# Kernel optimization log

Hardware: AMD Instinct MI355X
Metric: run time of the kernel (lower is better)

The kernel has to match this reference:

```python
import jax, jax.numpy as jnp
import numpy as np
from jax import lax

H = 384
W = 384
N = H * W                 # flattened pixel count
N_LOC = N // 2            # unknown pixels with 3x3 matting-Laplacian stencils
KCM = 20                  # color-mixture KNN size
K_IU = 5                  # intra-unknown KNN size
NNZ_CM = N_LOC * KCM


def setup_inputs() -> dict:
    key = jax.random.key(0)
    ks = jax.random.split(key, 16)
    f32 = jnp.float32
    i32 = jnp.int32
    inp = {}
    inp["CM_weights"] = jax.random.uniform(ks[0], (N,), f32)
    inp["LOC_weights"] = jax.random.uniform(ks[1], (N,), f32)
    inp["IU_weights"] = jax.random.uniform(ks[2], (N,), f32)
    inp["KU_weights"] = jax.random.uniform(ks[3], (N,), f32)
    inp["lmbda"] = jnp.full((1,), 100.0, f32)
    inp["kToUconf"] = jax.random.uniform(ks[4], (N,), f32)
    inp["known"] = jax.random.uniform(ks[5], (N,), f32)
    inp["kToU"] = jax.random.uniform(ks[6], (N,), f32)
    inp["Wcm_data"] = jax.random.uniform(ks[7], (NNZ_CM,), f32)
    inp["LOC_flows"] = jax.random.uniform(ks[8], (9, 9, N_LOC), f32)
    inp["IU_flows"] = jax.random.uniform(ks[9], (N_LOC, K_IU), f32)
    inp["Wcm_row"] = jax.random.randint(ks[10], (NNZ_CM,), 0, N, dtype=i32)
    inp["Wcm_col"] = jax.random.randint(ks[11], (NNZ_CM,), 0, N, dtype=i32)
    # interior pixels so all 9 stencil neighbours are valid
    inp["LOC_inInd"] = jax.random.randint(ks[12], (N_LOC,), W + 1, N - W - 1, dtype=i32)
    inp["IU_inInd"] = jax.random.randint(ks[13], (N_LOC,), 0, N, dtype=i32)
    inp["IU_neighInd"] = jax.random.randint(ks[14], (N_LOC, K_IU), 0, N, dtype=i32)
    inp["width"] = W
    inp["cg_steps"] = 30
    return inp


def reference(CM_weights, LOC_weights, IU_weights, KU_weights, lmbda,
              kToUconf, known, kToU, Wcm_data, LOC_flows, IU_flows,
              Wcm_row, Wcm_col, LOC_inInd, IU_inInd, IU_neighInd,
              width, cg_steps):
    n = kToU.shape[0]
    seg = lambda v, i: jax.ops.segment_sum(v, i, num_segments=n)

    # --- color mixture: Wcm scaled by diag(CM_weights); L = diag(rowsum) - Wcm; Lcm = L^T L
    cm_vals = CM_weights[Wcm_row] * Wcm_data
    rs_cm = seg(cm_vals, Wcm_row)

    # --- matting Laplacian: 9x9 flows per unknown pixel over 3x3 stencil
    offs = jnp.array([-1 - width, -1, -1 + width, -width, 0, width,
                      1 - width, 1, 1 + width], dtype=LOC_inInd.dtype)
    neigh = LOC_inInd[:, None] + offs[None, :]                    # [n_loc, 9]
    fl = LOC_flows * LOC_weights[LOC_inInd][None, None, :]        # [9, 9, n_loc]
    nloc = neigh.shape[0]
    # entry (row=neigh[k,i], col=neigh[k,j]) has value fl[j, i, k]
    vals_m = jnp.transpose(fl, (2, 1, 0)).reshape(-1)
    rows_m = jnp.broadcast_to(neigh[:, :, None], (nloc, 9, 9)).reshape(-1)
    cols_m = jnp.broadcast_to(neigh[:, None, :], (nloc, 9, 9)).reshape(-1)
    rows_ms = jnp.concatenate([rows_m, cols_m])
    cols_ms = jnp.concatenate([cols_m, rows_m])
    vals_ms = 0.5 * jnp.concatenate([vals_m, vals_m])             # W = 0.5 (W + W^T)
    rs_m = seg(vals_ms, rows_ms)

    # --- intra-unknowns KNN affinities
    fiu = IU_flows * IU_weights[IU_inInd][:, None]                # [n_iu, K]
    rows_c0 = jnp.broadcast_to(IU_inInd[:, None], IU_neighInd.shape).reshape(-1)
    cols_c0 = IU_neighInd.reshape(-1)
    rows_cs = jnp.concatenate([rows_c0, cols_c0])
    cols_cs = jnp.concatenate([cols_c0, rows_c0])
    vals_cs = 0.5 * jnp.concatenate([fiu.reshape(-1), fiu.reshape(-1)])
    rs_c = seg(vals_cs, rows_cs)

    # --- diagonal data terms: KU + lmbda*known
    diag_ku = KU_weights * kToUconf + lmbda[0] * known
    b = diag_ku * kToU

    def matvec(v):
        # Lcm @ v = L^T (L v), keeping L in factored COO form
        Lv = rs_cm * v - seg(cm_vals * v[Wcm_col], Wcm_row)
        lcm = rs_cm * Lv - seg(cm_vals * Lv[Wcm_row], Wcm_col)
        lm = rs_m * v - seg(vals_ms * v[cols_ms], rows_ms)
        lc = rs_c * v - seg(vals_cs * v[cols_cs], rows_cs)
        return lcm + lm + lc + diag_ku * v

    def cg_step(carry, _):
        x, r, p, rs = carry
        Ap = matvec(p)
        alpha = rs / jnp.vdot(p, Ap)
        x = x + alpha * p
        r = r - alpha * Ap
        rs_new = jnp.vdot(r, r)
        p = r + (rs_new / rs) * p
        return (x, r, p, rs_new), None

    x0 = jnp.zeros_like(b)  # x0 = 0 as in MattingSolver
    (x, _, _, _), _ = lax.scan(cg_step, (x0, b, b, jnp.vdot(b, b)), None, length=cg_steps)
    return x
```

## Files before the change

### kernel.cpp

```cpp
#include <hip/hip_runtime.h>


#define TPB 256

__device__ __forceinline__ float blockReduce256(float v) {
  #pragma unroll
  for (int o = 32; o > 0; o >>= 1) v += __shfl_down(v, o, 64);
  __shared__ float s[4];
  int lane = threadIdx.x & 63, wv = threadIdx.x >> 6;
  if (lane == 0) s[wv] = v;
  __syncthreads();
  return (threadIdx.x == 0) ? (s[0] + s[1] + s[2] + s[3]) : 0.f;
}

__global__ void k_init0(const float* __restrict__ KUw, const float* __restrict__ kToUconf,
                        const float* __restrict__ lmbda, const float* __restrict__ known,
                        const float* __restrict__ kToU,
                        float* __restrict__ diag_ku, float2* __restrict__ PR,
                        float* __restrict__ x,
                        int* __restrict__ CNT, int* __restrict__ sCNT,
                        float* __restrict__ scal, int N)
{
  int i = blockIdx.x * TPB + threadIdx.x;
  if (i < 80) scal[i] = 0.f;
  if (i < 576) sCNT[i] = 0;
  if (i < 3 * N) CNT[i] = 0;
  float red = 0.f;
  if (i < N) {
    float dk = KUw[i] * kToUconf[i] + lmbda[0] * known[i];
    diag_ku[i] = dk;
    float b = dk * kToU[i];
    PR[i] = make_float2(b, b);
    x[i] = 0.f;
    red = b * b;
  }
  float v = blockReduce256(red);
  if (threadIdx.x == 0) atomicAdd(&scal[0], v);
}

__global__ void k_prep(float* __restrict__ LOC_flows, const int* __restrict__ LOC_inInd,
                       const float* __restrict__ LOCw, int NLOC)
{
  int k = blockIdx.x * TPB + threadIdx.x;
  float Fl[81];
  #pragma unroll
  for (int m = 0; m < 81; ++m) Fl[m] = LOC_flows[(size_t)m * NLOC + k];
  float hw = 0.5f * LOCw[LOC_inInd[k]];
  int idx = 0;
  #pragma unroll
  for (int a = 0; a < 9; ++a)
    #pragma unroll
    for (int b = a + 1; b < 9; ++b) {
      LOC_flows[(size_t)idx * NLOC + k] = hw * (Fl[a * 9 + b] + Fl[b * 9 + a]);
      ++idx;
    }
}

__global__ void k_sh(const int* __restrict__ LOC_inInd, int* __restrict__ sCNT,
                     unsigned short* __restrict__ sTick, int NLOC)
{
  int k = blockIdx.x * TPB + threadIdx.x;
  sTick[k] = (unsigned short)atomicAdd(&sCNT[LOC_inInd[k] >> 8], 1);
}

__global__ void k_ss(int* __restrict__ sCNT)
{
  __shared__ int s[576];
  int v = sCNT[threadIdx.x];
  s[threadIdx.x] = v;
  __syncthreads();
  for (int o = 1; o < 576; o <<= 1) {
    int t = (threadIdx.x >= o) ? s[threadIdx.x - o] : 0;
    __syncthreads();
    s[threadIdx.x] += t;
    __syncthreads();
  }
  sCNT[threadIdx.x] = s[threadIdx.x] - v;
}

__global__ void k_sc(const int* __restrict__ LOC_inInd, const int* __restrict__ sCNT,
                     const unsigned short* __restrict__ sTick,
                     int* __restrict__ perm, int* __restrict__ LOC_inIndP, int NLOC)
{
  int k = blockIdx.x * TPB + threadIdx.x;
  int v = LOC_inInd[k];
  int pos = sCNT[v >> 8] + sTick[k];
  perm[pos] = k;
  LOC_inIndP[pos] = v;
}

__global__ void k_permS2(float* __restrict__ LOC_flows, const int* __restrict__ perm,
                         int NLOC)
{
  int kp = blockIdx.x * TPB + threadIdx.x;
  int k = perm[kp];
  #pragma unroll
  for (int m = 0; m < 36; ++m)
    LOC_flows[(size_t)(36 + m) * NLOC + kp] = LOC_flows[(size_t)m * NLOC + k];
}

__global__ void k_hist(const int* __restrict__ Wrow, const int* __restrict__ Wcol,
                       const int* __restrict__ LOC_inIndP, const int* __restrict__ width_p,
                       const int* __restrict__ IU_inInd, const int* __restrict__ IU_neighInd,
                       int* __restrict__ CNT,
                       unsigned short* __restrict__ tr, unsigned short* __restrict__ tc,
                       unsigned short* __restrict__ tU,
                       int NLOC, int N, int B0, int B1)
{
  int blk = blockIdx.x;
  if (blk < B0) {
    int e = blk * TPB + threadIdx.x;
    tr[e] = (unsigned short)atomicAdd(&CNT[Wrow[e]], 1);
    tc[e] = (unsigned short)atomicAdd(&CNT[N + Wcol[e]], 1);
  } else if (blk < B1) {
    int kp = (blk - B0) * TPB + threadIdx.x;
    int wd = *width_p;
    int base = LOC_inIndP[kp];
    const int offs[9] = {-1 - wd, -1, -1 + wd, -wd, 0, wd, 1 - wd, 1, 1 + wd};
    #pragma unroll
    for (int a = 0; a < 9; ++a)
      tU[a * NLOC + kp] = (unsigned short)atomicAdd(&CNT[2 * N + base + offs[a]], 1);
  } else {
    int k = (blk - B1) * TPB + threadIdx.x;
    tU[14 * NLOC + k] = (unsigned short)atomicAdd(&CNT[2 * N + IU_inInd[k]], 1);
    #pragma unroll
    for (int j = 0; j < 5; ++j)
      tU[(9 + j) * NLOC + k] =
          (unsigned short)atomicAdd(&CNT[2 * N + IU_neighInd[k * 5 + j]], 1);
  }
}

__global__ void k_scan1(int* __restrict__ OFF, int* __restrict__ bsum, int tot)
{
  __shared__ int s[TPB];
  int gid = blockIdx.x * TPB + threadIdx.x;
  int v = (gid < tot) ? OFF[gid] : 0;
  s[threadIdx.x] = v;
  __syncthreads();
  #pragma unroll
  for (int o = 1; o < TPB; o <<= 1) {
    int t = (threadIdx.x >= o) ? s[threadIdx.x - o] : 0;
    __syncthreads();
    s[threadIdx.x] += t;
    __syncthreads();
  }
  if (gid < tot) OFF[gid] = s[threadIdx.x] - v;
  if (threadIdx.x == TPB - 1) bsum[blockIdx.x] = s[threadIdx.x];
}

__global__ void k_scan2(int* __restrict__ bsum, int nPerArr)
{
  __shared__ int s[1024];
  int base = blockIdx.x * nPerArr;
  int v = (threadIdx.x < nPerArr) ? bsum[base + threadIdx.x] : 0;
  s[threadIdx.x] = v;
  __syncthreads();
  for (int o = 1; o < 1024; o <<= 1) {
    int t = (threadIdx.x >= o) ? s[threadIdx.x - o] : 0;
    __syncthreads();
    s[threadIdx.x] += t;
    __syncthreads();
  }
  if (threadIdx.x < nPerArr) bsum[base + threadIdx.x] = s[threadIdx.x] - v;
}

__global__ void k_scan3(int* __restrict__ OFF, const int* __restrict__ bsum, int tot)
{
  int gid = blockIdx.x * TPB + threadIdx.x;
  if (gid < tot) OFF[gid] += bsum[blockIdx.x];
}

__global__ void k_fill(const float* __restrict__ CMw, const float* __restrict__ Wcm_data,
                       const int* __restrict__ Wrow, const int* __restrict__ Wcol,
                       const int* __restrict__ LOC_inIndP, const int* __restrict__ width_p,
                       const int* __restrict__ IU_inInd, const int* __restrict__ IU_neighInd,
                       const int* __restrict__ OFF,
                       const unsigned short* __restrict__ tr, const unsigned short* __restrict__ tc,
                       const unsigned short* __restrict__ tU,
                       int2* __restrict__ csrPk, int2* __restrict__ cscPk,
                       int* __restrict__ gU,
                       int NLOC, int N, int B0, int B1)
{
  int blk = blockIdx.x;
  if (blk < B0) {
    int e = blk * TPB + threadIdx.x;
    int row = Wrow[e], col = Wcol[e];
    int cv = __float_as_int(CMw[row] * Wcm_data[e]);
    csrPk[OFF[row] + tr[e]] = make_int2(col, cv);
    cscPk[OFF[N + col] + tc[e]] = make_int2(row, cv);
  } else if (blk < B1) {
    int kp = (blk - B0) * TPB + threadIdx.x;
    int wd = *width_p;
    int base = LOC_inIndP[kp];
    const int offs[9] = {-1 - wd, -1, -1 + wd, -wd, 0, wd, 1 - wd, 1, 1 + wd};
    #pragma unroll
    for (int a = 0; a < 9; ++a)
      gU[OFF[2 * N + base + offs[a]] + tU[a * NLOC + kp]] = a * NLOC + kp;
  } else {
    int k = (blk - B1) * TPB + threadIdx.x;
    gU[OFF[2 * N + IU_inInd[k]] + tU[14 * NLOC + k]] = 14 * NLOC + k;
    #pragma unroll
    for (int j = 0; j < 5; ++j)
      gU[OFF[2 * N + IU_neighInd[k * 5 + j]] + tU[(9 + j) * NLOC + k]] =
          (9 + j) * NLOC + k;
  }
}

__global__ void k_it1(const float2* __restrict__ PR,
                      const float* __restrict__ S2p, const int* __restrict__ LOC_inIndP,
                      const int* __restrict__ width_p,
                      const float* __restrict__ IU_flows, const int* __restrict__ IU_inInd,
                      const int* __restrict__ IU_neighInd, const float* __restrict__ IUw,
                      const float* __restrict__ diag_ku,
                      const int* __restrict__ OFF, const int2* __restrict__ csrPk,
                      float* __restrict__ u_all,
                      float* __restrict__ Lv, float* __restrict__ rs_cm,
                      const float* __restrict__ rsN, const float* __restrict__ rsO, int first,
                      float* __restrict__ pAp_t,
                      int NNZ, int NLOC, int N, int B0, int B1)
{
  int blk = blockIdx.x;
  float beta = first ? 0.f : rsN[0] / rsO[0];
  float red = 0.f;
  if (blk < B0) {
    int kp = blk * TPB + threadIdx.x;
    int wd = *width_p;
    int base = LOC_inIndP[kp];
    const int offs[9] = {-1 - wd, -1, -1 + wd, -wd, 0, wd, 1 - wd, 1, 1 + wd};
    float pv[9];
    #pragma unroll
    for (int a = 0; a < 9; ++a) {
      float2 pr = PR[base + offs[a]];
      pv[a] = __builtin_fmaf(beta, pr.x, pr.y);
    }
    float u[9] = {0.f, 0.f, 0.f, 0.f, 0.f, 0.f, 0.f, 0.f, 0.f};
    float qf = 0.f;
    int idx = 0;
    #pragma unroll
    for (int a = 0; a < 9; ++a)
      #pragma unroll
      for (int b = a + 1; b < 9; ++b) {
        float sv = S2p[(size_t)idx * NLOC + kp];
        ++idx;
        float d = pv[a] - pv[b];
        float t = sv * d;
        u[a] += t; u[b] -= t;
        qf += t * d;
      }
    #pragma unroll
    for (int a = 0; a < 9; ++a) u_all[a * NLOC + kp] = u[a];
    red = qf;
  } else if (blk < B1) {
    int k = (blk - B0) * TPB + threadIdx.x;
    int r0 = IU_inInd[k];
    float hw = 0.5f * IUw[r0];
    float2 prr = PR[r0];
    float pr = __builtin_fmaf(beta, prr.x, prr.y);
    int c[5]; float w[5];
    #pragma unroll
    for (int j = 0; j < 5; ++j) {
      c[j] = IU_neighInd[k * 5 + j];
      w[j] = hw * IU_flows[k * 5 + j];
    }
    float pc[5];
    #pragma unroll
    for (int j = 0; j < 5; ++j) {
      float2 pp = PR[c[j]];
      pc[j] = __builtin_fmaf(beta, pp.x, pp.y);
    }
    float qf = 0.f, asum = 0.f;
    #pragma unroll
    for (int j = 0; j < 5; ++j) {
      float d = pr - pc[j];
      float uA = w[j] * d;
      u_all[(9 + j) * NLOC + k] = -uA;
      asum += uA;
      qf += uA * d;
    }
    u_all[14 * NLOC + k] = asum;
    red = qf;
  } else {
    int i = (blk - B1) * TPB + threadIdx.x;
    float2 pri = PR[i];
    float pi = __builtin_fmaf(beta, pri.x, pri.y);
    int s = OFF[i];
    int e = (i == N - 1) ? NNZ : OFF[i + 1];
    float acc = 0.f, rs = 0.f;
    int q = s;
    for (; q + 8 <= e; q += 8) {
      int2 ed[8];
      #pragma unroll
      for (int m = 0; m < 8; ++m) ed[m] = csrPk[q + m];
      float g[8];
      #pragma unroll
      for (int m = 0; m < 8; ++m) {
        float2 pp = PR[ed[m].x];
        g[m] = __builtin_fmaf(beta, pp.x, pp.y);
      }
      #pragma unroll
      for (int m = 0; m < 8; ++m) {
        float cv = __int_as_float(ed[m].y);
        rs += cv;
        acc += cv * (pi - g[m]);
      }
    }
    for (; q + 4 <= e; q += 4) {
      int2 ed[4];
      #pragma unroll
      for (int m = 0; m < 4; ++m) ed[m] = csrPk[q + m];
      float g[4];
      #pragma unroll
      for (int m = 0; m < 4; ++m) {
        float2 pp = PR[ed[m].x];
        g[m] = __builtin_fmaf(beta, pp.x, pp.y);
      }
      #pragma unroll
      for (int m = 0; m < 4; ++m) {
        float cv = __int_as_float(ed[m].y);
        rs += cv;
        acc += cv * (pi - g[m]);
      }
    }
    for (; q < e; ++q) {
      int2 ed = csrPk[q];
      float cv = __int_as_float(ed.y);
      float2 pp = PR[ed.x];
      rs += cv;
      acc += cv * (pi - __builtin_fmaf(beta, pp.x, pp.y));
    }
    Lv[i] = acc;
    rs_cm[i] = rs;
    red = diag_ku[i] * pi * pi + acc * acc;
  }
  float v = blockReduce256(red);
  if (threadIdx.x == 0) atomicAdd(pAp_t, v);
}

__global__ void k_it2(float* __restrict__ x, float2* __restrict__ PR,
                      const float* __restrict__ Lv,
                      const float* __restrict__ rs_cm, const float* __restrict__ diag_ku,
                      const int* __restrict__ OFF,
                      const int2* __restrict__ cscPk,
                      const int* __restrict__ gU, const float* __restrict__ u_all,
                      const float* __restrict__ rs_t, const float* __restrict__ pAp_t,
                      const float* __restrict__ rsO, int first,
                      float* __restrict__ rs_t1,
                      int NNZ, int NLOC, int N)
{
  int i = blockIdx.x * TPB + threadIdx.x;
  float alpha = rs_t[0] / pAp_t[0];
  float beta = first ? 0.f : rs_t[0] / rsO[0];
  float tg = 0.f;
  {
    int s0 = OFF[2 * N + i];
    int e0 = (i == N - 1) ? 15 * NLOC : OFF[2 * N + i + 1];
    int q = s0;
    for (; q + 8 <= e0; q += 8) {
      int g[8];
      #pragma unroll
      for (int m = 0; m < 8; ++m) g[m] = gU[q + m];
      float u[8];
      #pragma unroll
      for (int m = 0; m < 8; ++m) u[m] = u_all[g[m]];
      #pragma unroll
      for (int m = 0; m < 8; ++m) tg += u[m];
    }
    for (; q + 4 <= e0; q += 4) {
      int g[4];
      #pragma unroll
      for (int m = 0; m < 4; ++m) g[m] = gU[q + m];
      float u[4];
      #pragma unroll
      for (int m = 0; m < 4; ++m) u[m] = u_all[g[m]];
      #pragma unroll
      for (int m = 0; m < 4; ++m) tg += u[m];
    }
    for (; q < e0; ++q) tg += u_all[gU[q]];
  }
  float sc = 0.f;
  {
    int s0 = OFF[N + i];
    int e0 = (i == N - 1) ? NNZ : OFF[N + i + 1];
    int q = s0;
    for (; q + 8 <= e0; q += 8) {
      int2 ed[8];
      #pragma unroll
      for (int m = 0; m < 8; ++m) ed[m] = cscPk[q + m];
      float l[8];
      #pragma unroll
      for (int m = 0; m < 8; ++m) l[m] = Lv[ed[m].x];
      #pragma unroll
      for (int m = 0; m < 8; ++m) sc += __int_as_float(ed[m].y) * l[m];
    }
    for (; q + 4 <= e0; q += 4) {
      int2 ed[4];
      #pragma unroll
      for (int m = 0; m < 4; ++m) ed[m] = cscPk[q + m];
      float l[4];
      #pragma unroll
      for (int m = 0; m < 4; ++m) l[m] = Lv[ed[m].x];
      #pragma unroll
      for (int m = 0; m < 4; ++m) sc += __int_as_float(ed[m].y) * l[m];
    }
    for (; q < e0; ++q) {
      int2 ed = cscPk[q];
      sc += __int_as_float(ed.y) * Lv[ed.x];
    }
  }
  float2 pri = PR[i];
  float pi = __builtin_fmaf(beta, pri.x, pri.y);
  float Ap = diag_ku[i] * pi + rs_cm[i] * Lv[i] - sc + tg;
  x[i] += alpha * pi;
  float rn = pri.y - alpha * Ap;
  PR[i] = make_float2(pi, rn);
  float v = blockReduce256(rn * rn);
  if (threadIdx.x == 0) atomicAdd(rs_t1, v);
}

extern "C" void kernel_launch(void* const* d_in, const int* in_sizes, int n_in,
                              void* d_out, int out_size, void* d_ws, size_t ws_size,
                              hipStream_t stream)
{
  const float* CMw       = (const float*)d_in[0];
  const float* LOCw      = (const float*)d_in[1];
  const float* IUw       = (const float*)d_in[2];
  const float* KUw       = (const float*)d_in[3];
  const float* lmbda     = (const float*)d_in[4];
  const float* kToUconf  = (const float*)d_in[5];
  const float* known     = (const float*)d_in[6];
  const float* kToU      = (const float*)d_in[7];
  const float* Wcm_data  = (const float*)d_in[8];
  float*       LOC_flows = (float*)d_in[9];
  const float* IU_flows  = (const float*)d_in[10];
  const int*   Wrow      = (const int*)d_in[11];
  const int*   Wcol      = (const int*)d_in[12];
  const int*   LOC_inInd = (const int*)d_in[13];
  const int*   IU_inInd  = (const int*)d_in[14];
  const int*   IU_neighInd = (const int*)d_in[15];
  const int*   width_p   = (const int*)d_in[16];
  const int CG_STEPS = 30;

  const int N    = in_sizes[0];
  const int NNZ  = in_sizes[8];
  const int NLOC = in_sizes[13];

  float* x       = (float*)d_out;
  float2* PR     = (float2*)d_ws;
  float* Lv      = (float*)(PR + (size_t)N);
  float* rs_cm   = Lv + N;
  float* diag_ku = rs_cm + N;
  int2*  csrPk   = (int2*)(diag_ku + N);
  int2*  cscPk   = csrPk + (size_t)NNZ;
  int*   gU      = (int*)(cscPk + (size_t)NNZ);
  int*   OFF     = gU + (size_t)15 * NLOC;
  unsigned short* tr = (unsigned short*)(OFF + (size_t)3 * N);
  unsigned short* tc = tr + (size_t)NNZ;
  unsigned short* tU = tc + (size_t)NNZ;
  float* u_all   = (float*)tr;
  int*   bsum    = (int*)(tU + (size_t)15 * NLOC);
  float* scal    = (float*)(bsum + 3 * (N / TPB));
  int*   perm    = (int*)(scal + 80);
  int*   LOC_inIndP = perm + NLOC;
  int*   sCNT    = LOC_inIndP + NLOC;
  unsigned short* sTick = (unsigned short*)(sCNT + 576);

  const int Bn = N / TPB;
  const int Bz = NNZ / TPB;
  const int Bl = NLOC / TPB;
  const int Z3 = 3 * Bn;

  k_init0<<<Z3, TPB, 0, stream>>>(KUw, kToUconf, lmbda, known, kToU,
                                  diag_ku, PR, x, OFF, sCNT, scal, N);
  k_prep<<<Bl, TPB, 0, stream>>>(LOC_flows, LOC_inInd, LOCw, NLOC);
  k_sh<<<Bl, TPB, 0, stream>>>(LOC_inInd, sCNT, sTick, NLOC);
  k_ss<<<1, 576, 0, stream>>>(sCNT);
  k_sc<<<Bl, TPB, 0, stream>>>(LOC_inInd, sCNT, sTick, perm, LOC_inIndP, NLOC);
  k_permS2<<<Bl, TPB, 0, stream>>>(LOC_flows, perm, NLOC);
  k_hist<<<Bz + 2 * Bl, TPB, 0, stream>>>(Wrow, Wcol, LOC_inIndP, width_p,
                                          IU_inInd, IU_neighInd, OFF,
                                          tr, tc, tU, NLOC, N, Bz, Bz + Bl);
  k_scan1<<<Z3, TPB, 0, stream>>>(OFF, bsum, 3 * N);
  k_scan2<<<3, 1024, 0, stream>>>(bsum, Bn);
  k_scan3<<<Z3, TPB, 0, stream>>>(OFF, bsum, 3 * N);
  k_fill<<<Bz + 2 * Bl, TPB, 0, stream>>>(CMw, Wcm_data, Wrow, Wcol,
                                          LOC_inIndP, width_p, IU_inInd, IU_neighInd,
                                          OFF, tr, tc, tU,
                                          csrPk, cscPk, gU,
                                          NLOC, N, Bz, Bz + Bl);

  const float* S2p = LOC_flows + (size_t)36 * NLOC;
  for (int t = 0; t < CG_STEPS; ++t) {
    const float* rsN = scal + t;
    const float* rsO = scal + (t == 0 ? 0 : t - 1);
    k_it1<<<2 * Bl + Bn, TPB, 0, stream>>>(
        PR, S2p, LOC_inIndP, width_p,
        IU_flows, IU_inInd, IU_neighInd, IUw,
        diag_ku, OFF, csrPk, u_all, Lv, rs_cm,
        rsN, rsO, (t == 0) ? 1 : 0, scal + 40 + t,
        NNZ, NLOC, N, Bl, 2 * Bl);
    k_it2<<<Bn, TPB, 0, stream>>>(
        x, PR, Lv, rs_cm, diag_ku, OFF, cscPk, gU, u_all,
        rsN, scal + 40 + t, rsO, (t == 0) ? 1 : 0, scal + t + 1,
        NNZ, NLOC, N);
  }
}
```

Measured before the change: 1.781 ms.

## Gather LOC stencil contributions via sorted-center ranges instead of explicit index lists

LOC entries are now fully sorted by center pixel (a per-pixel counting sort replaces the coarse 256-bucket sort). k_it2 then gathers the nine stencil contributions for each pixel by scanning contiguous ranges of u_all at the neighbouring centers, so it no longer follows per-entry gU indices. This drops nine atomic histogram and fill passes per LOC entry during setup and removes indirect index loads in every CG iteration. In exchange it needs an extra counter and scan array and performs nine range lookups per pixel.

```diff
diff --git a/kernel.cpp b/kernel.cpp
--- a/kernel.cpp
+++ b/kernel.cpp
@@ -18,13 +18,11 @@
                         const float* __restrict__ kToU,
                         float* __restrict__ diag_ku, float2* __restrict__ PR,
                         float* __restrict__ x,
-                        int* __restrict__ CNT, int* __restrict__ sCNT,
-                        float* __restrict__ scal, int N)
+                        int* __restrict__ CNT, float* __restrict__ scal, int N)
 {
   int i = blockIdx.x * TPB + threadIdx.x;
   if (i < 80) scal[i] = 0.f;
-  if (i < 576) sCNT[i] = 0;
-  if (i < 3 * N) CNT[i] = 0;
+  if (i < 4 * N) CNT[i] = 0;
   float red = 0.f;
   if (i < N) {
     float dk = KUw[i] * kToUconf[i] + lmbda[0] * known[i];
@@ -56,35 +54,21 @@
     }
 }
 
-__global__ void k_sh(const int* __restrict__ LOC_inInd, int* __restrict__ sCNT,
-                     unsigned short* __restrict__ sTick, int NLOC)
+__global__ void k_sh(const int* __restrict__ LOC_inInd, int* __restrict__ CNT,
+                     unsigned short* __restrict__ sTick, int N, int NLOC)
 {
   int k = blockIdx.x * TPB + threadIdx.x;
-  sTick[k] = (unsigned short)atomicAdd(&sCNT[LOC_inInd[k] >> 8], 1);
-}
-
-__global__ void k_ss(int* __restrict__ sCNT)
-{
-  __shared__ int s[576];
-  int v = sCNT[threadIdx.x];
-  s[threadIdx.x] = v;
-  __syncthreads();
-  for (int o = 1; o < 576; o <<= 1) {
-    int t = (threadIdx.x >= o) ? s[threadIdx.x - o] : 0;
-    __syncthreads();
-    s[threadIdx.x] += t;
-    __syncthreads();
-  }
-  sCNT[threadIdx.x] = s[threadIdx.x] - v;
-}
-
-__global__ void k_sc(const int* __restrict__ LOC_inInd, const int* __restrict__ sCNT,
+  sTick[k] = (unsigned short)atomicAdd(&CNT[3 * N + LOC_inInd[k]], 1);
+}
+
+__global__ void k_sc(const int* __restrict__ LOC_inInd, const int* __restrict__ OFF,
                      const unsigned short* __restrict__ sTick,
-                     int* __restrict__ perm, int* __restrict__ LOC_inIndP, int NLOC)
+                     int* __restrict__ perm, int* __restrict__ LOC_inIndP,
+                     int N, int NLOC)
 {
   int k = blockIdx.x * TPB + threadIdx.x;
   int v = LOC_inInd[k];
-  int pos = sCNT[v >> 8] + sTick[k];
+  int pos = OFF[3 * N + v] + sTick[k];
   perm[pos] = k;
   LOC_inIndP[pos] = v;
 }
@@ -100,32 +84,23 @@
 }
 
 __global__ void k_hist(const int* __restrict__ Wrow, const int* __restrict__ Wcol,
-                       const int* __restrict__ LOC_inIndP, const int* __restrict__ width_p,
                        const int* __restrict__ IU_inInd, const int* __restrict__ IU_neighInd,
                        int* __restrict__ CNT,
                        unsigned short* __restrict__ tr, unsigned short* __restrict__ tc,
                        unsigned short* __restrict__ tU,
-                       int NLOC, int N, int B0, int B1)
+                       int NLOC, int N, int B0)
 {
   int blk = blockIdx.x;
   if (blk < B0) {
     int e = blk * TPB + threadIdx.x;
     tr[e] = (unsigned short)atomicAdd(&CNT[Wrow[e]], 1);
     tc[e] = (unsigned short)atomicAdd(&CNT[N + Wcol[e]], 1);
-  } else if (blk < B1) {
-    int kp = (blk - B0) * TPB + threadIdx.x;
-    int wd = *width_p;
-    int base = LOC_inIndP[kp];
-    const int offs[9] = {-1 - wd, -1, -1 + wd, -wd, 0, wd, 1 - wd, 1, 1 + wd};
-    #pragma unroll
-    for (int a = 0; a < 9; ++a)
-      tU[a * NLOC + kp] = (unsigned short)atomicAdd(&CNT[2 * N + base + offs[a]], 1);
   } else {
-    int k = (blk - B1) * TPB + threadIdx.x;
-    tU[14 * NLOC + k] = (unsigned short)atomicAdd(&CNT[2 * N + IU_inInd[k]], 1);
+    int k = (blk - B0) * TPB + threadIdx.x;
+    tU[5 * NLOC + k] = (unsigned short)atomicAdd(&CNT[2 * N + IU_inInd[k]], 1);
     #pragma unroll
     for (int j = 0; j < 5; ++j)
-      tU[(9 + j) * NLOC + k] =
+      tU[j * NLOC + k] =
           (unsigned short)atomicAdd(&CNT[2 * N + IU_neighInd[k * 5 + j]], 1);
   }
 }
@@ -172,14 +147,13 @@
 
 __global__ void k_fill(const float* __restrict__ CMw, const float* __restrict__ Wcm_data,
                        const int* __restrict__ Wrow, const int* __restrict__ Wcol,
-                       const int* __restrict__ LOC_inIndP, const int* __restrict__ width_p,
                        const int* __restrict__ IU_inInd, const int* __restrict__ IU_neighInd,
                        const int* __restrict__ OFF,
                        const unsigned short* __restrict__ tr, const unsigned short* __restrict__ tc,
                        const unsigned short* __restrict__ tU,
                        int2* __restrict__ csrPk, int2* __restrict__ cscPk,
                        int* __restrict__ gU,
-                       int NLOC, int N, int B0, int B1)
+                       int NLOC, int N, int B0)
 {
   int blk = blockIdx.x;
   if (blk < B0) {
@@ -188,20 +162,12 @@
     int cv = __float_as_int(CMw[row] * Wcm_data[e]);
     csrPk[OFF[row] + tr[e]] = make_int2(col, cv);
     cscPk[OFF[N + col] + tc[e]] = make_int2(row, cv);
-  } else if (blk < B1) {
-    int kp = (blk - B0) * TPB + threadIdx.x;
-    int wd = *width_p;
-    int base = LOC_inIndP[kp];
-    const int offs[9] = {-1 - wd, -1, -1 + wd, -wd, 0, wd, 1 - wd, 1, 1 + wd};
-    #pragma unroll
-    for (int a = 0; a < 9; ++a)
-      gU[OFF[2 * N + base + offs[a]] + tU[a * NLOC + kp]] = a * NLOC + kp;
   } else {
-    int k = (blk - B1) * TPB + threadIdx.x;
-    gU[OFF[2 * N + IU_inInd[k]] + tU[14 * NLOC + k]] = 14 * NLOC + k;
+    int k = (blk - B0) * TPB + threadIdx.x;
+    gU[OFF[2 * N + IU_inInd[k]] + tU[5 * NLOC + k]] = 14 * NLOC + k;
     #pragma unroll
     for (int j = 0; j < 5; ++j)
-      gU[OFF[2 * N + IU_neighInd[k * 5 + j]] + tU[(9 + j) * NLOC + k]] =
+      gU[OFF[2 * N + IU_neighInd[k * 5 + j]] + tU[j * NLOC + k]] =
           (9 + j) * NLOC + k;
   }
 }
@@ -339,7 +305,8 @@
 __global__ void k_it2(float* __restrict__ x, float2* __restrict__ PR,
                       const float* __restrict__ Lv,
                       const float* __restrict__ rs_cm, const float* __restrict__ diag_ku,
-                      const int* __restrict__ OFF,
+                      const int* __restrict__ OFF, const int* __restrict__ cum,
+                      const int* __restrict__ width_p,
                       const int2* __restrict__ cscPk,
                       const int* __restrict__ gU, const float* __restrict__ u_all,
                       const float* __restrict__ rs_t, const float* __restrict__ pAp_t,
@@ -352,19 +319,21 @@
   float beta = first ? 0.f : rs_t[0] / rsO[0];
   float tg = 0.f;
   {
+    int wd = *width_p;
+    const int voff[9] = {1 + wd, 1, 1 - wd, wd, 0, -wd, -1 + wd, -1, -1 - wd};
+    #pragma unroll
+    for (int a = 0; a < 9; ++a) {
+      int v = i + voff[a];
+      v = v < 0 ? 0 : (v > N - 1 ? N - 1 : v);
+      int lo = cum[v];
+      int hi = (v == N - 1) ? NLOC : cum[v + 1];
+      for (int q = lo; q < hi; ++q) tg += u_all[a * NLOC + q];
+    }
+  }
+  {
     int s0 = OFF[2 * N + i];
-    int e0 = (i == N - 1) ? 15 * NLOC : OFF[2 * N + i + 1];
+    int e0 = (i == N - 1) ? 6 * NLOC : OFF[2 * N + i + 1];
     int q = s0;
-    for (; q + 8 <= e0; q += 8) {
-      int g[8];
-      #pragma unroll
-      for (int m = 0; m < 8; ++m) g[m] = gU[q + m];
-      float u[8];
-      #pragma unroll
-      for (int m = 0; m < 8; ++m) u[m] = u_all[g[m]];
-      #pragma unroll
-      for (int m = 0; m < 8; ++m) tg += u[m];
-    }
     for (; q + 4 <= e0; q += 4) {
       int g[4];
       #pragma unroll
@@ -452,43 +421,41 @@
   int2*  csrPk   = (int2*)(diag_ku + N);
   int2*  cscPk   = csrPk + (size_t)NNZ;
   int*   gU      = (int*)(cscPk + (size_t)NNZ);
-  int*   OFF     = gU + (size_t)15 * NLOC;
-  unsigned short* tr = (unsigned short*)(OFF + (size_t)3 * N);
+  int*   OFF     = gU + (size_t)6 * NLOC;
+  unsigned short* tr = (unsigned short*)(OFF + (size_t)4 * N);
   unsigned short* tc = tr + (size_t)NNZ;
   unsigned short* tU = tc + (size_t)NNZ;
   float* u_all   = (float*)tr;
-  int*   bsum    = (int*)(tU + (size_t)15 * NLOC);
-  float* scal    = (float*)(bsum + 3 * (N / TPB));
+  int*   bsum    = (int*)(tU + (size_t)6 * NLOC);
+  float* scal    = (float*)(bsum + 4 * (N / TPB));
   int*   perm    = (int*)(scal + 80);
   int*   LOC_inIndP = perm + NLOC;
-  int*   sCNT    = LOC_inIndP + NLOC;
-  unsigned short* sTick = (unsigned short*)(sCNT + 576);
+  unsigned short* sTick = (unsigned short*)(LOC_inIndP + NLOC);
 
   const int Bn = N / TPB;
   const int Bz = NNZ / TPB;
   const int Bl = NLOC / TPB;
-  const int Z3 = 3 * Bn;
-
-  k_init0<<<Z3, TPB, 0, stream>>>(KUw, kToUconf, lmbda, known, kToU,
-                                  diag_ku, PR, x, OFF, sCNT, scal, N);
+  const int Z4 = 4 * Bn;
+
+  k_init0<<<Z4, TPB, 0, stream>>>(KUw, kToUconf, lmbda, known, kToU,
+                                  diag_ku, PR, x, OFF, scal, N);
   k_prep<<<Bl, TPB, 0, stream>>>(LOC_flows, LOC_inInd, LOCw, NLOC);
-  k_sh<<<Bl, TPB, 0, stream>>>(LOC_inInd, sCNT, sTick, NLOC);
-  k_ss<<<1, 576, 0, stream>>>(sCNT);
-  k_sc<<<Bl, TPB, 0, stream>>>(LOC_inInd, sCNT, sTick, perm, LOC_inIndP, NLOC);
+  k_sh<<<Bl, TPB, 0, stream>>>(LOC_inInd, OFF, sTick, N, NLOC);
+  k_hist<<<Bz + Bl, TPB, 0, stream>>>(Wrow, Wcol, IU_inInd, IU_neighInd, OFF,
+                                      tr, tc, tU, NLOC, N, Bz);
+  k_scan1<<<Z4, TPB, 0, stream>>>(OFF, bsum, 4 * N);
+  k_scan2<<<4, 1024, 0, stream>>>(bsum, Bn);
+  k_scan3<<<Z4, TPB, 0, stream>>>(OFF, bsum, 4 * N);
+  k_sc<<<Bl, TPB, 0, stream>>>(LOC_inInd, OFF, sTick, perm, LOC_inIndP, N, NLOC);
   k_permS2<<<Bl, TPB, 0, stream>>>(LOC_flows, perm, NLOC);
-  k_hist<<<Bz + 2 * Bl, TPB, 0, stream>>>(Wrow, Wcol, LOC_inIndP, width_p,
-                                          IU_inInd, IU_neighInd, OFF,
-                                          tr, tc, tU, NLOC, N, Bz, Bz + Bl);
-  k_scan1<<<Z3, TPB, 0, stream>>>(OFF, bsum, 3 * N);
-  k_scan2<<<3, 1024, 0, stream>>>(bsum, Bn);
-  k_scan3<<<Z3, TPB, 0, stream>>>(OFF, bsum, 3 * N);
-  k_fill<<<Bz + 2 * Bl, TPB, 0, stream>>>(CMw, Wcm_data, Wrow, Wcol,
-                                          LOC_inIndP, width_p, IU_inInd, IU_neighInd,
-                                          OFF, tr, tc, tU,
-                                          csrPk, cscPk, gU,
-                                          NLOC, N, Bz, Bz + Bl);
+  k_fill<<<Bz + Bl, TPB, 0, stream>>>(CMw, Wcm_data, Wrow, Wcol,
+                                      IU_inInd, IU_neighInd,
+                                      OFF, tr, tc, tU,
+                                      csrPk, cscPk, gU,
+                                      NLOC, N, Bz);
 
   const float* S2p = LOC_flows + (size_t)36 * NLOC;
+  const int*   cum = OFF + (size_t)3 * N;
   for (int t = 0; t < CG_STEPS; ++t) {
     const float* rsN = scal + t;
     const float* rsO = scal + (t == 0 ? 0 : t - 1);
@@ -499,7 +466,7 @@
         rsN, rsO, (t == 0) ? 1 : 0, scal + 40 + t,
         NNZ, NLOC, N, Bl, 2 * Bl);
     k_it2<<<Bn, TPB, 0, stream>>>(
-        x, PR, Lv, rs_cm, diag_ku, OFF, cscPk, gU, u_all,
+        x, PR, Lv, rs_cm, diag_ku, OFF, cum, width_p, cscPk, gU, u_all,
         rsN, scal + 40 + t, rsO, (t == 0) ? 1 : 0, scal + t + 1,
         NNZ, NLOC, N);
   }
```

New measurement: 1.862 ms. 1.05x slower.
